# Performance work log

Hardware: AMD Instinct MI355X
Metric: run time of the kernel (lower is better)

## Reference

```python
import jax, jax.numpy as jnp
import numpy as np

D_MODEL = 1024
NUM_HEADS = 16
D_K = D_MODEL // NUM_HEADS
D_FF = 4096
LN_EPS = 1e-5


def layer_norm(x, gamma, beta):
    mu = jnp.mean(x, axis=-1, keepdims=True)
    var = jnp.var(x, axis=-1, keepdims=True)
    return (x - mu) * jax.lax.rsqrt(var + LN_EPS) * gamma + beta


def setup_inputs() -> dict:
    key = jax.random.key(0)
    ks = jax.random.split(key, 10)
    s = 0.02
    return {
        "x": jax.random.normal(ks[0], (2, 2048, D_MODEL), dtype=jnp.float32),
        # per-head projections stacked: [H, d_model, d_k] (equivalent to the
        # num_heads separate nn.Linear(d_model, d_k, bias=False) modules)
        "Wq": jax.random.normal(ks[1], (NUM_HEADS, D_MODEL, D_K), dtype=jnp.float32) * s,
        "Wk": jax.random.normal(ks[2], (NUM_HEADS, D_MODEL, D_K), dtype=jnp.float32) * s,
        "Wv": jax.random.normal(ks[3], (NUM_HEADS, D_MODEL, D_K), dtype=jnp.float32) * s,
        "Wo": jax.random.normal(ks[4], (D_MODEL, D_MODEL), dtype=jnp.float32) * s,
        "W1": jax.random.normal(ks[5], (D_MODEL, D_FF), dtype=jnp.float32) * s,
        "b1": jnp.zeros((D_FF,), dtype=jnp.float32),
        "W2": jax.random.normal(ks[6], (D_FF, D_MODEL), dtype=jnp.float32) * s,
        "b2": jnp.zeros((D_MODEL,), dtype=jnp.float32),
        "g1": jnp.ones((D_MODEL,), dtype=jnp.float32),
        "beta1": jnp.zeros((D_MODEL,), dtype=jnp.float32),
        "g2": jnp.ones((D_MODEL,), dtype=jnp.float32),
        "beta2": jnp.zeros((D_MODEL,), dtype=jnp.float32),
    }


def reference(x, Wq, Wk, Wv, Wo, W1, b1, W2, b2, g1, beta1, g2, beta2):
    B, S, D = x.shape
    # ---- pre-LN multi-head self-attention ----
    h = layer_norm(x, g1, beta1)
    # batched QKV projections (equivalent to the per-head Python loop)
    Q = jnp.einsum('bsd,hdk->bhsk', h, Wq)  # [B,H,S,dk]
    K = jnp.einsum('bsd,hdk->bhsk', h, Wk)
    V = jnp.einsum('bsd,hdk->bhsk', h, Wv)
    scores = jnp.einsum('bhqk,bhsk->bhqs', Q, K) / jnp.sqrt(jnp.asarray(D_K, x.dtype))
    weights = jax.nn.softmax(scores, axis=-1)  # [B,H,S,S]
    attn = jnp.einsum('bhqs,bhsk->bhqk', weights, V)  # [B,H,S,dk]
    # concat heads along feature dim (head order preserved)
    concat = attn.transpose(0, 2, 1, 3).reshape(B, S, D)
    x = x + concat @ Wo
    # ---- pre-LN FFN (exact erf GELU, matching nn.GELU default) ----
    h2 = layer_norm(x, g2, beta2)
    ffn = jax.nn.gelu(h2 @ W1 + b1, approximate=False) @ W2 + b2
    return x + ffn
```

## Files before the change

kernel.cpp:

```cpp
#include <hip/hip_runtime.h>
#include <stdint.h>


typedef __attribute__((ext_vector_type(8))) short bf16x8;
typedef __attribute__((ext_vector_type(4))) float f32x4;
typedef __attribute__((ext_vector_type(16))) float f32x16;
typedef __attribute__((ext_vector_type(4))) unsigned short u16x4;
typedef __attribute__((ext_vector_type(4))) unsigned int u32x4;

#define DEV __device__ __forceinline__

static constexpr int DM   = 1024;
static constexpr int DFF  = 4096;
static constexpr int NH   = 16;
static constexpr int DKH  = 64;
static constexpr int SEQ  = 2048;
static constexpr int NBAT = 2;
static constexpr int NTOK = NBAT * SEQ;

DEV unsigned short f2bf(float f) {
  union { float f; unsigned int u; } v; v.f = f;
  unsigned int u = v.u;
  return (unsigned short)((u + 0x7fffu + ((u >> 16) & 1u)) >> 16);
}

DEV void gload_lds16(const unsigned short* g, unsigned short* l) {
  __builtin_amdgcn_global_load_lds(
      (const __attribute__((address_space(1))) unsigned int*)g,
      (__attribute__((address_space(3))) unsigned int*)l, 16, 0, 0);
}

DEV float fast_gelu(float x) {
  const float z = fabsf(x) * 0.70710678118654752f;
  const float t = __builtin_amdgcn_rcpf(1.0f + 0.3275911f * z);
  float p = 1.061405429f;
  p = p * t - 1.453152027f;
  p = p * t + 1.421413741f;
  p = p * t - 0.284496736f;
  p = p * t + 0.254829592f;
  p = p * t;
  float erfv = 1.0f - p * __expf(-z * z);
  erfv = copysignf(erfv, x);
  return 0.5f * x * (1.0f + erfv);
}

__global__ __launch_bounds__(256) void ln_kernel(
    const float* __restrict__ x, const float* __restrict__ g,
    const float* __restrict__ be, unsigned short* __restrict__ out) {
  const int row = blockIdx.x;
  const int t = threadIdx.x;
  const int lane = t & 63, w = t >> 6;
  const float4* xr = (const float4*)(x + (size_t)row * DM);
  float4 v = xr[t];
  float s  = v.x + v.y + v.z + v.w;
  float s2 = v.x * v.x + v.y * v.y + v.z * v.z + v.w * v.w;
#pragma unroll
  for (int off = 32; off; off >>= 1) {
    s  += __shfl_down(s, off);
    s2 += __shfl_down(s2, off);
  }
  __shared__ float rs_[4], rq_[4];
  if (lane == 0) { rs_[w] = s; rq_[w] = s2; }
  __syncthreads();
  float fs = rs_[0] + rs_[1] + rs_[2] + rs_[3];
  float fq = rq_[0] + rq_[1] + rq_[2] + rq_[3];
  float mu = fs * (1.0f / DM);
  float var = fq * (1.0f / DM) - mu * mu;
  float rstd = rsqrtf(var + 1e-5f);
  float4 gv = ((const float4*)g)[t];
  float4 bv = ((const float4*)be)[t];
  u16x4 o;
  o[0] = f2bf((v.x - mu) * rstd * gv.x + bv.x);
  o[1] = f2bf((v.y - mu) * rstd * gv.y + bv.y);
  o[2] = f2bf((v.z - mu) * rstd * gv.z + bv.z);
  o[3] = f2bf((v.w - mu) * rstd * gv.w + bv.w);
  *(u16x4*)(out + (size_t)row * DM + t * 4) = o;
}

__global__ __launch_bounds__(256) void convert_weights(
    const float* __restrict__ Wq, const float* __restrict__ Wk,
    const float* __restrict__ Wv, const float* __restrict__ Wo,
    const float* __restrict__ W1, const float* __restrict__ W2,
    unsigned short* __restrict__ wqkv_t, unsigned short* __restrict__ wo_t,
    unsigned short* __restrict__ w1_t, unsigned short* __restrict__ w2_t) {
  const int NQKV = 3 * DM * DM;
  const int NWO  = DM * DM;
  const int NW1  = DM * DFF;
  const int NW2  = DM * DFF;
  const int total = NQKV + NWO + NW1 + NW2;
  for (int idx = blockIdx.x * 256 + threadIdx.x; idx < total;
       idx += gridDim.x * 256) {
    if (idx < NQKV) {
      int n = idx >> 10, d = idx & 1023;
      int which = n >> 10, nn = n & 1023, h = nn >> 6, kk = nn & 63;
      const float* W = (which == 0) ? Wq : (which == 1) ? Wk : Wv;
      wqkv_t[idx] = f2bf(W[((h << 10) + d) * 64 + kk]);
    } else if (idx < NQKV + NWO) {
      int i = idx - NQKV;
      int n = i >> 10, d = i & 1023;
      wo_t[i] = f2bf(Wo[(d << 10) + n]);
    } else if (idx < NQKV + NWO + NW1) {
      int i = idx - NQKV - NWO;
      int n = i >> 10, d = i & 1023;
      w1_t[i] = f2bf(W1[d * DFF + n]);
    } else {
      int i = idx - NQKV - NWO - NW1;
      int n = i >> 12, s = i & 4095;
      w2_t[i] = f2bf(W2[s * DM + n]);
    }
  }
}

struct EpiArgs {
  unsigned short* q;
  unsigned short* k;
  unsigned short* vt;
  unsigned short* ob16;
  float* of32;
  float* p0;
  const float* bias;
  const float* resid;
};

template <int EPI>
DEV void epilogue_elem(float v, int row, int col, int N, int bz,
                       const EpiArgs& ep) {
  if constexpr (EPI == 0) {
    const int bb = row >> 11, rr = row & 2047;
    if (col < 1024) {
      const int hh = col >> 6, dk = col & 63;
      const int kk = dk >> 4, h8 = (dk >> 3) & 1, e = dk & 7;
      const int qblk = rr >> 5, l31 = rr & 31;
      ep.q[((size_t)(bb * NH + hh) * 64 + qblk) * 2048 + kk * 512 +
           (h8 * 32 + l31) * 8 + e] = f2bf(v * 0.125f);
    } else if (col < 2048) {
      const int c = col - 1024;
      const int hh = c >> 6, dk = c & 63;
      const int kk = dk >> 4, h8 = (dk >> 3) & 1, e = dk & 7;
      const int kvblk = rr >> 5, l31 = rr & 31;
      ep.k[((size_t)(bb * NH + hh) * 64 + kvblk) * 2048 + kk * 512 +
           (h8 * 32 + l31) * 8 + e] = f2bf(v);
    } else {
      const int c = col - 2048, hh = c >> 6, dd = c & 63;
      const int ssw = (rr & ~12) | ((rr & 4) << 1) | ((rr & 8) >> 1);
      const int t64 = ssw >> 6, w = (ssw >> 4) & 3;
      const int h8 = (ssw >> 3) & 1, e = ssw & 7;
      const int dblk = dd >> 5, l31 = dd & 31;
      ep.vt[(((size_t)(bb * NH + hh) * 32 + t64) * 8 + dblk * 4 + w) * 512 +
            (h8 * 32 + l31) * 8 + e] = f2bf(v);
    }
  } else if constexpr (EPI == 1) {
    const size_t idx = (size_t)row * N + col;
    ep.of32[idx] = v + ep.resid[idx];
  } else if constexpr (EPI == 2) {
    ep.ob16[(size_t)row * N + col] = f2bf(fast_gelu(v + ep.bias[col]));
  } else {
    const size_t idx = (size_t)row * N + col;
    if (bz == 0) ep.p0[idx] = v;
    else ep.of32[idx] = ep.of32[idx] + v + ep.bias[col];
  }
}

template <int EPI>
__global__ __launch_bounds__(256) void gemm_pipe(
    const unsigned short* __restrict__ A, const unsigned short* __restrict__ Bt,
    int N, int Kc, int ldk, EpiArgs ep) {
  __shared__ __align__(16) unsigned short Als[2][128 * 64];
  __shared__ __align__(16) unsigned short Bls[2][128 * 64];
  const int t = threadIdx.x, lane = t & 63, wave = t >> 6;
  const int wm = wave >> 1, wn = wave & 1;
  const int g = lane >> 4, r16 = lane & 15;
  const int m0 = blockIdx.y * 128, n0 = blockIdx.x * 128;
  const int kbase = blockIdx.z * Kc;

  f32x4 acc[4][4];
  const f32x4 z4 = {0.f, 0.f, 0.f, 0.f};
#pragma unroll
  for (int i = 0; i < 4; ++i)
#pragma unroll
    for (int j = 0; j < 4; ++j) acc[i][j] = z4;

  auto stage = [&](int b, int k0) {
#pragma unroll
    for (int i = 0; i < 4; ++i) {
      const int cb = i * 256 + wave * 64;
      const int c = cb + lane;
      const int row = c >> 3;
      const int sc = ((c & 7) ^ (row & 7)) * 8;
      gload_lds16(A + (size_t)(m0 + row) * ldk + kbase + k0 + sc, &Als[b][cb * 8]);
      gload_lds16(Bt + (size_t)(n0 + row) * ldk + kbase + k0 + sc, &Bls[b][cb * 8]);
    }
  };

  const int NT = Kc >> 6;
  stage(0, 0);
  __syncthreads();
  for (int kt = 0; kt < NT; ++kt) {
    const int cur = kt & 1;
    if (kt + 1 < NT) stage(cur ^ 1, (kt + 1) << 6);
    const int sw = r16 & 7;
    bf16x8 af[2][4], bfr[2][4];
#pragma unroll
    for (int ks = 0; ks < 2; ++ks) {
#pragma unroll
      for (int mt = 0; mt < 4; ++mt)
        af[ks][mt] = *(const bf16x8*)&Als[cur][(wm * 64 + mt * 16 + r16) * 64 +
                                              (((ks << 2) | g) ^ sw) * 8];
#pragma unroll
      for (int nt = 0; nt < 4; ++nt)
        bfr[ks][nt] = *(const bf16x8*)&Bls[cur][(wn * 64 + nt * 16 + r16) * 64 +
                                               (((ks << 2) | g) ^ sw) * 8];
    }
    __builtin_amdgcn_s_setprio(1);
#pragma unroll
    for (int ks = 0; ks < 2; ++ks)
#pragma unroll
      for (int mt = 0; mt < 4; ++mt)
#pragma unroll
        for (int nt = 0; nt < 4; ++nt)
          acc[mt][nt] = __builtin_amdgcn_mfma_f32_16x16x32_bf16(
              af[ks][mt], bfr[ks][nt], acc[mt][nt], 0, 0, 0);
    __builtin_amdgcn_s_setprio(0);
    __syncthreads();
  }
#pragma unroll
  for (int mt = 0; mt < 4; ++mt)
#pragma unroll
    for (int nt = 0; nt < 4; ++nt)
#pragma unroll
      for (int r = 0; r < 4; ++r)
        epilogue_elem<EPI>(acc[mt][nt][r], m0 + wm * 64 + mt * 16 + g * 4 + r,
                           n0 + wn * 64 + nt * 16 + r16, N, blockIdx.z, ep);
}

__global__ __launch_bounds__(256) void reduce_add(const float* __restrict__ p,
                                                  float* __restrict__ out) {
  const int i = blockIdx.x * 256 + threadIdx.x;
  float4 a = ((const float4*)p)[i];
  float4 b = ((float4*)out)[i];
  b.x += a.x; b.y += a.y; b.z += a.z; b.w += a.w;
  ((float4*)out)[i] = b;
}

struct AttnState {
  f32x16 o0, o1;
  float m, lsum;
};

DEV void load_k(const unsigned short* kbase, int s, bf16x8 k0[4], bf16x8 k1[4]) {
  const unsigned short* p = kbase + (size_t)(s >> 5) * 2048;
#pragma unroll
  for (int kk = 0; kk < 4; ++kk) {
    k0[kk] = *(const bf16x8*)(p + kk * 512);
    k1[kk] = *(const bf16x8*)(p + 2048 + kk * 512);
  }
}

DEV void attn_tile(const bf16x8 k0[4], const bf16x8 k1[4],
                   const bf16x8 v0[4], const bf16x8 v1[4],
                   const bf16x8 qf[4], AttnState& st) {
  const f32x16 z16 = {0.f};
  f32x16 pA = z16, pB = z16;
  __builtin_amdgcn_s_setprio(1);
#pragma unroll
  for (int kk = 0; kk < 4; ++kk) {
    pA = __builtin_amdgcn_mfma_f32_32x32x16_bf16(k0[kk], qf[kk], pA, 0, 0, 0);
    pB = __builtin_amdgcn_mfma_f32_32x32x16_bf16(k1[kk], qf[kk], pB, 0, 0, 0);
  }
  __builtin_amdgcn_s_setprio(0);
  float m0 = fmaxf(pA[0], pB[0]), m1 = fmaxf(pA[1], pB[1]);
  float m2 = fmaxf(pA[2], pB[2]), m3 = fmaxf(pA[3], pB[3]);
#pragma unroll
  for (int r = 4; r < 16; r += 4) {
    m0 = fmaxf(m0, fmaxf(pA[r + 0], pB[r + 0]));
    m1 = fmaxf(m1, fmaxf(pA[r + 1], pB[r + 1]));
    m2 = fmaxf(m2, fmaxf(pA[r + 2], pB[r + 2]));
    m3 = fmaxf(m3, fmaxf(pA[r + 3], pB[r + 3]));
  }
  float mx = fmaxf(fmaxf(m0, m1), fmaxf(m2, m3));
  mx = fmaxf(mx, __shfl_xor(mx, 32));
  if (__any(mx > st.m + 8.f)) {
    const float mnew = fmaxf(st.m, mx);
    const float corr = __expf(st.m - mnew);
#pragma unroll
    for (int r = 0; r < 16; ++r) { st.o0[r] *= corr; st.o1[r] *= corr; }
    st.lsum *= corr;
    st.m = mnew;
  }
  float ps = 0.f;
#pragma unroll
  for (int r = 0; r < 16; ++r) {
    pA[r] = __expf(pA[r] - st.m); ps += pA[r];
    pB[r] = __expf(pB[r] - st.m); ps += pB[r];
  }
  ps += __shfl_xor(ps, 32);
  st.lsum += ps;
  bf16x8 pw[4];
#pragma unroll
  for (int w = 0; w < 4; ++w) {
    unsigned int wd0, wd1, wd2, wd3;
    const int e0 = (w & 1) * 8;
    if (w < 2) {
      asm("v_cvt_pk_bf16_f32 %0, %1, %2" : "=v"(wd0) : "v"(pA[e0 + 0]), "v"(pA[e0 + 1]));
      asm("v_cvt_pk_bf16_f32 %0, %1, %2" : "=v"(wd1) : "v"(pA[e0 + 2]), "v"(pA[e0 + 3]));
      asm("v_cvt_pk_bf16_f32 %0, %1, %2" : "=v"(wd2) : "v"(pA[e0 + 4]), "v"(pA[e0 + 5]));
      asm("v_cvt_pk_bf16_f32 %0, %1, %2" : "=v"(wd3) : "v"(pA[e0 + 6]), "v"(pA[e0 + 7]));
    } else {
      asm("v_cvt_pk_bf16_f32 %0, %1, %2" : "=v"(wd0) : "v"(pB[e0 + 0]), "v"(pB[e0 + 1]));
      asm("v_cvt_pk_bf16_f32 %0, %1, %2" : "=v"(wd1) : "v"(pB[e0 + 2]), "v"(pB[e0 + 3]));
      asm("v_cvt_pk_bf16_f32 %0, %1, %2" : "=v"(wd2) : "v"(pB[e0 + 4]), "v"(pB[e0 + 5]));
      asm("v_cvt_pk_bf16_f32 %0, %1, %2" : "=v"(wd3) : "v"(pB[e0 + 6]), "v"(pB[e0 + 7]));
    }
    u32x4 wv = {wd0, wd1, wd2, wd3};
    pw[w] = __builtin_bit_cast(bf16x8, wv);
  }
  __builtin_amdgcn_s_setprio(1);
#pragma unroll
  for (int w = 0; w < 4; ++w) {
    st.o0 = __builtin_amdgcn_mfma_f32_32x32x16_bf16(v0[w], pw[w], st.o0, 0, 0, 0);
    st.o1 = __builtin_amdgcn_mfma_f32_32x32x16_bf16(v1[w], pw[w], st.o1, 0, 0, 0);
  }
  __builtin_amdgcn_s_setprio(0);
}

__global__ __launch_bounds__(256, 2) void attn_kernel(
    const unsigned short* __restrict__ Qc, const unsigned short* __restrict__ Kc,
    const unsigned short* __restrict__ Vt, unsigned short* __restrict__ Oc) {
  const int lane = threadIdx.x & 63, wave = threadIdx.x >> 6;
  const int hi = lane >> 5, l31 = lane & 31;
  const int i = blockIdx.x;
  const int k8 = i & 7, mq = i >> 3;
  const int grp = k8 + 8 * (mq >> 4);
  const int qb = mq & 15;
  const int b = grp >> 4, h = grp & 15;
  const int q0 = qb * 128 + wave * 32;

  const unsigned short* qbp = Qc + ((size_t)grp * 64 + (q0 >> 5)) * 2048 + lane * 8;
  const unsigned short* kbp = Kc + (size_t)grp * 64 * 2048 + lane * 8;
  const unsigned short* vbp = Vt + (size_t)grp * 32 * 4096 + lane * 8;

  bf16x8 qf[4];
#pragma unroll
  for (int kk = 0; kk < 4; ++kk) qf[kk] = *(const bf16x8*)(qbp + kk * 512);

  AttnState st;
#pragma unroll
  for (int r = 0; r < 16; ++r) { st.o0[r] = 0.f; st.o1[r] = 0.f; }
  st.m = -1e30f; st.lsum = 0.f;

  bf16x8 kA0[4], kA1[4], kB0[4], kB1[4];
  load_k(kbp, 0, kA0, kA1);

  for (int s0 = 0; s0 < SEQ; s0 += 128) {
    const unsigned short* vt0 = vbp + (size_t)(s0 >> 6) * 4096;
    bf16x8 v0[4], v1[4];
#pragma unroll
    for (int w = 0; w < 4; ++w) {
      v0[w] = *(const bf16x8*)(vt0 + w * 512);
      v1[w] = *(const bf16x8*)(vt0 + 2048 + w * 512);
    }
    load_k(kbp, s0 + 64, kB0, kB1);
    attn_tile(kA0, kA1, v0, v1, qf, st);
    const unsigned short* vt1 = vbp + (size_t)((s0 + 64) >> 6) * 4096;
#pragma unroll
    for (int w = 0; w < 4; ++w) {
      v0[w] = *(const bf16x8*)(vt1 + w * 512);
      v1[w] = *(const bf16x8*)(vt1 + 2048 + w * 512);
    }
    const int snext = (s0 + 128 < SEQ) ? (s0 + 128) : 0;
    load_k(kbp, snext, kA0, kA1);
    attn_tile(kB0, kB1, v0, v1, qf, st);
  }

  const float inv = 1.0f / st.lsum;
  const size_t rowbase = (size_t)b * SEQ;
  unsigned short* op = Oc + (rowbase + q0 + l31) * DM + h * DKH + hi * 4;
#pragma unroll
  for (int dblk = 0; dblk < 2; ++dblk)
#pragma unroll
    for (int g4 = 0; g4 < 4; ++g4) {
      u16x4 stv;
#pragma unroll
      for (int r = 0; r < 4; ++r) {
        const float v = (dblk ? st.o1[g4 * 4 + r] : st.o0[g4 * 4 + r]) * inv;
        stv[r] = f2bf(v);
      }
      *(u16x4*)(op + dblk * 32 + g4 * 8) = stv;
    }
}

extern "C" void kernel_launch(void* const* d_in, const int* in_sizes, int n_in,
                              void* d_out, int out_size, void* d_ws,
                              size_t ws_size, hipStream_t stream) {
  (void)in_sizes; (void)n_in; (void)out_size; (void)ws_size;
  const float* x   = (const float*)d_in[0];
  const float* Wq  = (const float*)d_in[1];
  const float* Wk  = (const float*)d_in[2];
  const float* Wv  = (const float*)d_in[3];
  const float* Wo  = (const float*)d_in[4];
  const float* W1  = (const float*)d_in[5];
  const float* b1  = (const float*)d_in[6];
  const float* W2  = (const float*)d_in[7];
  const float* b2  = (const float*)d_in[8];
  const float* g1  = (const float*)d_in[9];
  const float* be1 = (const float*)d_in[10];
  const float* g2  = (const float*)d_in[11];
  const float* be2 = (const float*)d_in[12];
  float* out = (float*)d_out;

  char* ws = (char*)d_ws;
  const size_t MB = 1024 * 1024;
  unsigned short* h_buf  = (unsigned short*)(ws + 0 * MB);
  unsigned short* wqkv_t = (unsigned short*)(ws + 8 * MB);
  unsigned short* wo_t   = (unsigned short*)(ws + 14 * MB);
  unsigned short* w1_t   = (unsigned short*)(ws + 16 * MB);
  unsigned short* w2_t   = (unsigned short*)(ws + 24 * MB);
  unsigned short* q_attn = (unsigned short*)(ws + 32 * MB);
  unsigned short* k_attn = (unsigned short*)(ws + 40 * MB);
  unsigned short* v_attn = (unsigned short*)(ws + 48 * MB);
  unsigned short* ffn1   = (unsigned short*)(ws + 32 * MB);
  float*          p0     = (float*)(ws + 0 * MB);

  EpiArgs e0 = {}; e0.q = q_attn; e0.k = k_attn; e0.vt = v_attn;
  EpiArgs e1 = {}; e1.of32 = out; e1.resid = x;
  EpiArgs e2 = {}; e2.ob16 = ffn1; e2.bias = b1;
  EpiArgs e4 = {}; e4.of32 = out; e4.p0 = p0; e4.bias = b2;

  convert_weights<<<12288, 256, 0, stream>>>(Wq, Wk, Wv, Wo, W1, W2,
                                             wqkv_t, wo_t, w1_t, w2_t);
  ln_kernel<<<NTOK, 256, 0, stream>>>(x, g1, be1, h_buf);
  gemm_pipe<0><<<dim3(3072 / 128, NTOK / 128, 1), 256, 0, stream>>>(
      h_buf, wqkv_t, 3072, DM, DM, e0);
  attn_kernel<<<512, 256, 0, stream>>>(q_attn, k_attn, v_attn, h_buf);
  gemm_pipe<1><<<dim3(DM / 128, NTOK / 128, 1), 256, 0, stream>>>(
      h_buf, wo_t, DM, DM, DM, e1);
  ln_kernel<<<NTOK, 256, 0, stream>>>(out, g2, be2, h_buf);
  gemm_pipe<2><<<dim3(DFF / 128, NTOK / 128, 1), 256, 0, stream>>>(
      h_buf, w1_t, DFF, DM, DM, e2);
  gemm_pipe<4><<<dim3(DM / 128, NTOK / 128, 2), 256, 0, stream>>>(
      ffn1, w2_t, DM, DFF / 2, DFF, e4);
  reduce_add<<<4096, 256, 0, stream>>>(p0, out);
}
```

Before: 300.0 us.

## Tile weight transpose through LDS and remap GEMM workgroups across XCDs

Replaces the strided element-wise weight conversion with a 64x64 LDS-tiled transpose, so both the fp32 reads and the bf16 writes are coalesced. The old kernel read transposed weights with large strides, which wasted memory bandwidth. The GEMM kernel also remaps workgroup IDs so that consecutive tiles land on the same XCD, aiming for better L2 reuse of A and B panels. The remap assumes the tile count is divisible by 8.

```diff
diff --git a/kernel.cpp b/kernel.cpp
--- a/kernel.cpp
+++ b/kernel.cpp
@@ -77,37 +77,47 @@
   *(u16x4*)(out + (size_t)row * DM + t * 4) = o;
 }
 
-__global__ __launch_bounds__(256) void convert_weights(
+__global__ __launch_bounds__(256) void transpose_weights(
     const float* __restrict__ Wq, const float* __restrict__ Wk,
     const float* __restrict__ Wv, const float* __restrict__ Wo,
     const float* __restrict__ W1, const float* __restrict__ W2,
     unsigned short* __restrict__ wqkv_t, unsigned short* __restrict__ wo_t,
     unsigned short* __restrict__ w1_t, unsigned short* __restrict__ w2_t) {
-  const int NQKV = 3 * DM * DM;
-  const int NWO  = DM * DM;
-  const int NW1  = DM * DFF;
-  const int NW2  = DM * DFF;
-  const int total = NQKV + NWO + NW1 + NW2;
-  for (int idx = blockIdx.x * 256 + threadIdx.x; idx < total;
-       idx += gridDim.x * 256) {
-    if (idx < NQKV) {
-      int n = idx >> 10, d = idx & 1023;
-      int which = n >> 10, nn = n & 1023, h = nn >> 6, kk = nn & 63;
-      const float* W = (which == 0) ? Wq : (which == 1) ? Wk : Wv;
-      wqkv_t[idx] = f2bf(W[((h << 10) + d) * 64 + kk]);
-    } else if (idx < NQKV + NWO) {
-      int i = idx - NQKV;
-      int n = i >> 10, d = i & 1023;
-      wo_t[i] = f2bf(Wo[(d << 10) + n]);
-    } else if (idx < NQKV + NWO + NW1) {
-      int i = idx - NQKV - NWO;
-      int n = i >> 10, d = i & 1023;
-      w1_t[i] = f2bf(W1[d * DFF + n]);
-    } else {
-      int i = idx - NQKV - NWO - NW1;
-      int n = i >> 12, s = i & 4095;
-      w2_t[i] = f2bf(W2[s * DM + n]);
-    }
+  __shared__ float lds[64][65];
+  const int t = blockIdx.x;
+  const float* inb; unsigned short* outb; int in_ld, out_ld;
+  if (t < 768) {
+    const int slice = t >> 4, tin = t & 15;
+    const int which = slice >> 4, h = slice & 15;
+    const float* W = (which == 0) ? Wq : (which == 1) ? Wk : Wv;
+    inb = W + (size_t)((h << 10) + (tin << 6)) * 64;
+    in_ld = 64;
+    outb = wqkv_t + ((size_t)((which << 10) + (h << 6)) << 10) + (tin << 6);
+    out_ld = 1024;
+  } else if (t < 1024) {
+    const int tt = t - 768, tr = tt >> 4, tc = tt & 15;
+    inb = Wo + (size_t)(tc << 6) * 1024 + (tr << 6); in_ld = 1024;
+    outb = wo_t + (size_t)(tr << 6) * 1024 + (tc << 6); out_ld = 1024;
+  } else if (t < 2048) {
+    const int tt = t - 1024, tr = tt >> 4, tc = tt & 15;
+    inb = W1 + (size_t)(tc << 6) * 4096 + (tr << 6); in_ld = 4096;
+    outb = w1_t + (size_t)(tr << 6) * 1024 + (tc << 6); out_ld = 1024;
+  } else {
+    const int tt = t - 2048, tr = tt >> 6, tc = tt & 63;
+    inb = W2 + (size_t)(tc << 6) * 1024 + (tr << 6); in_ld = 1024;
+    outb = w2_t + (size_t)(tr << 6) * 4096 + (tc << 6); out_ld = 4096;
+  }
+  const int j = threadIdx.x & 63, i0 = threadIdx.x >> 6;
+#pragma unroll
+  for (int p = 0; p < 16; ++p) {
+    const int i = i0 + p * 4;
+    lds[j][i] = inb[(size_t)i * in_ld + j];
+  }
+  __syncthreads();
+#pragma unroll
+  for (int p = 0; p < 16; ++p) {
+    const int r = i0 + p * 4;
+    outb[(size_t)r * out_ld + j] = f2bf(lds[r][j]);
   }
 }
 
@@ -170,7 +180,11 @@
   const int t = threadIdx.x, lane = t & 63, wave = t >> 6;
   const int wm = wave >> 1, wn = wave & 1;
   const int g = lane >> 4, r16 = lane & 15;
-  const int m0 = blockIdx.y * 128, n0 = blockIdx.x * 128;
+  const int nx = gridDim.x;
+  const int nwg = nx * gridDim.y;
+  int wgid = blockIdx.y * nx + blockIdx.x;
+  wgid = (wgid & 7) * (nwg >> 3) + (wgid >> 3);
+  const int m0 = (wgid / nx) * 128, n0 = (wgid % nx) * 128;
   const int kbase = blockIdx.z * Kc;
 
   f32x4 acc[4][4];
@@ -426,8 +440,8 @@
   EpiArgs e2 = {}; e2.ob16 = ffn1; e2.bias = b1;
   EpiArgs e4 = {}; e4.of32 = out; e4.p0 = p0; e4.bias = b2;
 
-  convert_weights<<<12288, 256, 0, stream>>>(Wq, Wk, Wv, Wo, W1, W2,
-                                             wqkv_t, wo_t, w1_t, w2_t);
+  transpose_weights<<<3072, 256, 0, stream>>>(Wq, Wk, Wv, Wo, W1, W2,
+                                              wqkv_t, wo_t, w1_t, w2_t);
   ln_kernel<<<NTOK, 256, 0, stream>>>(x, g1, be1, h_buf);
   gemm_pipe<0><<<dim3(3072 / 128, NTOK / 128, 1), 256, 0, stream>>>(
       h_buf, wqkv_t, 3072, DM, DM, e0);
```

Result: faster. 259.2 us (-13.6%).
